# Kernel optimization log

Hardware: AMD Instinct MI355X
Metric: run time of the kernel (lower is better)

## Reference

```python
import jax, jax.numpy as jnp
import numpy as np

B, IN, H, G, WR = 8192, 1024, 1024, 2, 64
UR = [64, 64]


def setup_inputs() -> dict:
    key = jax.random.key(0)
    ks = jax.random.split(key, 9)
    hg = H // G
    return {
        "x": jax.random.normal(ks[0], (B, IN), jnp.float32),
        "h": jax.random.normal(ks[1], (B, H), jnp.float32),
        "c": jax.random.normal(ks[2], (B, H), jnp.float32),
        "u_x": 0.1 * jax.random.normal(ks[3], (IN, WR), jnp.float32),
        "v_x": 0.1 * jax.random.normal(ks[4], (4 * H, WR), jnp.float32),
        "u_h_0": 0.1 * jax.random.normal(ks[5], (G, hg, UR[0]), jnp.float32),
        "v_h_0": 0.1 * jax.random.normal(ks[6], (G, UR[0], 4 * hg), jnp.float32),
        "u_h_1": 0.1 * jax.random.normal(ks[7], (G, hg, UR[1]), jnp.float32),
        "v_h_1": 0.1 * jax.random.normal(ks[8], (G, UR[1], 4 * hg), jnp.float32),
        "bias_x": jnp.ones((1, 4 * H), jnp.float32),
        "bias_h": jnp.ones((1, 4 * H), jnp.float32),
    }


def reference(x, h, c, u_x, v_x, u_h_0, v_h_0, u_h_1, v_h_1, bias_x, bias_h):
    b = h.shape[0]
    hg = H // G
    # input-to-hidden low-rank projection: [B, 4H]
    gx = (x @ u_x) @ v_x.T + bias_x
    xf, xi, xn, xo = jnp.split(gx, 4, axis=1)  # each [B, H]

    hv = h.reshape(b, G, hg)  # [B, G, H/G]
    u_hs = [u_h_0, u_h_1]
    v_hs = [v_h_0, v_h_1]
    acc = None
    for i in range(G):
        # torch code rotates the group index list cumulatively each step:
        # step i uses permutation roll(arange(G), -i)
        perm = np.roll(np.arange(G), -i)
        h_op = hv[:, perm, :]  # [B, G, hg]
        t = jnp.einsum('bgd,gdr->bgr', h_op, u_hs[i])  # [B, G, r_i]
        t = jnp.einsum('bgr,grk->bgk', t, v_hs[i])     # [B, G, 4hg]
        acc = t if acc is None else acc + t

    # chunk along last dim into 4 gates, flatten group dim -> [B, H]
    f_h, i_h, n_h, o_h = [p.reshape(b, H) for p in jnp.split(acc, 4, axis=2)]
    hf, hi, hn, ho = jnp.split(bias_h, 4, axis=1)

    inputgate = jax.nn.sigmoid(xi + hi + i_h)
    forgetgate = jax.nn.sigmoid(xf + hf + f_h)
    outputgate = jax.nn.sigmoid(xo + ho + o_h)
    newgate = jnp.tanh(xn + hn + n_h)
    c_next = forgetgate * c + inputgate * newgate
    h_next = outputgate * jnp.tanh(c_next)
    return (h_next, c_next)
```

## Files before the change

kernel.cpp:

```cpp
#include <hip/hip_runtime.h>
#include <hip/hip_bf16.h>


typedef __bf16 bf16_t;
typedef __bf16 bf16x4 __attribute__((ext_vector_type(4)));
typedef __bf16 bf16x8 __attribute__((ext_vector_type(8)));
typedef float f32x4 __attribute__((ext_vector_type(4)));

#define MFMA16x16x32(a, b, c) __builtin_amdgcn_mfma_f32_16x16x32_bf16((a), (b), (c), 0, 0, 0)

#define TA_OFF 0
#define BX_OFF 5242880
#define BH_OFF 5373952
#define BW_OFF 5636096

__device__ inline float fast_sigmoid(float x) {
  return __builtin_amdgcn_rcpf(1.f + __expf(-x));
}
__device__ inline float fast_tanh(float x) {
  return 2.f * __builtin_amdgcn_rcpf(1.f + __expf(-2.f * x)) - 1.f;
}

__global__ __launch_bounds__(256) void prep_kernel(
    const float* __restrict__ u_x, const float* __restrict__ u_h_0,
    const float* __restrict__ u_h_1, const float* __restrict__ v_h_0,
    const float* __restrict__ v_h_1, const float* __restrict__ v_x,
    bf16_t* __restrict__ Bx, bf16_t* __restrict__ Bh,
    bf16_t* __restrict__ Bw) {
  int o = blockIdx.x * 256 + threadIdx.x;
  if (o < 65536) {
    int j = o & 7, lane = (o >> 3) & 63, kk = (o >> 9) & 31, t = o >> 14;
    int lo = lane & 15, quad = lane >> 4;
    int k = kk * 32 + quad * 8 + j;
    Bx[o] = (bf16_t)u_x[k * 64 + 16 * t + lo];
  } else if (o < 196608) {
    int o2 = o - 65536;
    int j = o2 & 7, lane = (o2 >> 3) & 63, kk = (o2 >> 9) & 15;
    int sub = (o2 >> 13) & 3, s = o2 >> 15;
    int lo = lane & 15, quad = lane >> 4;
    int d = kk * 32 + quad * 8 + j;
    const float* src = (s & 1) ? u_h_1 : u_h_0;
    Bh[o2] = (bf16_t)src[(s >> 1) * 32768 + d * 64 + 16 * sub + lo];
  } else if (o < 983040) {
    int o3 = o - 196608;
    int j = o3 & 7, lane = (o3 >> 3) & 63;
    int chunk = o3 >> 9;
    int ks = chunk % 6, rowt = chunk / 6;
    int gq = rowt >> 3, nt = rowt & 7;
    int lo = lane & 15, quad = lane >> 4;
    int g = gq >> 4, qt = gq & 15;
    int row = 16 * nt + lo;
    int w = row >> 5, ql = row & 31;
    int k = ks * 32 + quad * 8 + j;
    int m = g * 512 + qt * 32 + ql;
    int q = qt * 32 + ql;
    float val;
    if (k < 64)
      val = v_x[(w * 1024 + m) * 64 + k];
    else if (k < 128)
      val = v_h_0[g * 131072 + (k - 64) * 2048 + w * 512 + q];
    else
      val = v_h_1[g * 131072 + (k - 128) * 2048 + w * 512 + q];
    Bw[o3] = (bf16_t)val;
  }
}

__global__ __launch_bounds__(256) void phase1_kernel(
    const float* __restrict__ x, const float* __restrict__ h,
    const bf16_t* __restrict__ Bx, const bf16_t* __restrict__ Bh,
    bf16_t* __restrict__ TA) {
  __shared__ bf16_t z[16][2072];
  __shared__ bf16_t pre[16][328];
  const int b0 = blockIdx.x * 16;
  const int tid = threadIdx.x;
  const int wv = tid >> 6, lane = tid & 63;
  const int lo = lane & 15, quad = lane >> 4;
  const int srow = tid >> 4, sc = tid & 15;

  {
    const float* srcx = x + (size_t)(b0 + srow) * 1024;
    const float* srch = h + (size_t)(b0 + srow) * 1024;
#pragma unroll
    for (int j = 0; j < 16; ++j) {
      int col = sc * 4 + j * 64;
      float4 v = *(const float4*)(srcx + col);
      bf16x4 pk;
      pk[0] = (bf16_t)v.x; pk[1] = (bf16_t)v.y;
      pk[2] = (bf16_t)v.z; pk[3] = (bf16_t)v.w;
      *(bf16x4*)&z[srow][col] = pk;
    }
#pragma unroll
    for (int j = 0; j < 16; ++j) {
      int col = sc * 4 + j * 64;
      float4 v = *(const float4*)(srch + col);
      bf16x4 pk;
      pk[0] = (bf16_t)v.x; pk[1] = (bf16_t)v.y;
      pk[2] = (bf16_t)v.z; pk[3] = (bf16_t)v.w;
      *(bf16x4*)&z[srow][1024 + col] = pk;
    }
  }
  __syncthreads();

  {
    f32x4 accx = {0.f, 0.f, 0.f, 0.f};
    const bf16_t* bx = Bx + ((size_t)(wv * 32) * 64 + lane) * 8;
    for (int kk = 0; kk < 32; ++kk) {
      bf16x8 af = *(const bf16x8*)&z[lo][kk * 32 + quad * 8];
      bf16x8 bfr = *(const bf16x8*)(bx + (size_t)kk * 512);
      accx = MFMA16x16x32(af, bfr, accx);
    }
#pragma unroll
    for (int r = 0; r < 4; ++r) pre[quad * 4 + r][16 * wv + lo] = (bf16_t)accx[r];
  }

  {
    const int hoff = 1024 + ((wv == 1 || wv == 2) ? 512 : 0);
    f32x4 acc[4];
#pragma unroll
    for (int sub = 0; sub < 4; ++sub) acc[sub] = (f32x4){0.f, 0.f, 0.f, 0.f};
    for (int kk = 0; kk < 16; ++kk) {
      bf16x8 af = *(const bf16x8*)&z[lo][hoff + kk * 32 + quad * 8];
#pragma unroll
      for (int sub = 0; sub < 4; ++sub) {
        bf16x8 bfr = *(const bf16x8*)(Bh +
            (((size_t)(wv * 4 + sub) * 16 + kk) * 64 + lane) * 8);
        acc[sub] = MFMA16x16x32(af, bfr, acc[sub]);
      }
    }
#pragma unroll
    for (int sub = 0; sub < 4; ++sub) {
      int n = 64 + wv * 64 + sub * 16 + lo;
#pragma unroll
      for (int r = 0; r < 4; ++r) pre[quad * 4 + r][n] = (bf16_t)acc[sub][r];
    }
  }
  __syncthreads();

#pragma unroll
  for (int it = 0; it < 3; ++it) {
    int slot = it * 256 + tid;
    if (slot < 640) {
      int cc = slot >> 6, ln = slot & 63;
      int llo = ln & 15, lq = ln >> 4;
      bf16x8 v = *(const bf16x8*)&pre[llo][cc * 32 + lq * 8];
      *(bf16x8*)(TA + (((size_t)blockIdx.x * 10 + cc) * 64 + ln) * 8) = v;
    }
  }
}

__global__ __launch_bounds__(256, 3) void phase2_kernel(
    const bf16_t* __restrict__ TA, const bf16_t* __restrict__ Bw,
    const float* __restrict__ bias_x, const float* __restrict__ bias_h,
    const float* __restrict__ c, float* __restrict__ out) {
  __shared__ bf16_t bs[3072 * 8];

  const int b0 = blockIdx.x * 128;
  const int gq = blockIdx.y;
  const int g = gq >> 4, qt = gq & 15;
  const int tid = threadIdx.x;
  const int wv = tid >> 6, lane = tid & 63;
  const int lo = lane & 15, quad = lane >> 4;

  bf16x8 a[2][6];
#pragma unroll
  for (int mt = 0; mt < 2; ++mt) {
    int rt = blockIdx.x * 8 + wv * 2 + mt;
#pragma unroll
    for (int ks = 0; ks < 6; ++ks) {
      int cc = (ks < 2) ? ks : (g * 4 + ks);
      a[mt][ks] = *(const bf16x8*)(TA + (((size_t)rt * 10 + cc) * 64 + lane) * 8);
    }
  }

  {
    const bf16_t* src = Bw + (size_t)gq * 24576;
#pragma unroll
    for (int cch = 0; cch < 12; ++cch) {
      int ch = cch * 256 + tid;
      *(bf16x8*)&bs[(size_t)ch * 8] = *(const bf16x8*)(src + (size_t)ch * 8);
    }
  }

  float cin[2][4][2];
#pragma unroll
  for (int mt = 0; mt < 2; ++mt)
#pragma unroll
    for (int r = 0; r < 4; ++r) {
      int b = b0 + wv * 32 + mt * 16 + quad * 4 + r;
#pragma unroll
      for (int cq = 0; cq < 2; ++cq) {
        int m = g * 512 + qt * 32 + cq * 16 + lo;
        cin[mt][r][cq] = c[(size_t)b * 1024 + m];
      }
    }
  float bsum[4][2];
#pragma unroll
  for (int w = 0; w < 4; ++w)
#pragma unroll
    for (int cq = 0; cq < 2; ++cq) {
      int n = w * 1024 + g * 512 + qt * 32 + cq * 16 + lo;
      bsum[w][cq] = bias_x[n] + bias_h[n];
    }
  __syncthreads();

  f32x4 acc[2][8];
#pragma unroll
  for (int mt = 0; mt < 2; ++mt)
#pragma unroll
    for (int nt = 0; nt < 8; ++nt) acc[mt][nt] = (f32x4){0.f, 0.f, 0.f, 0.f};

#pragma unroll
  for (int nt = 0; nt < 8; ++nt) {
#pragma unroll
    for (int ks = 0; ks < 6; ++ks) {
      bf16x8 bfr = *(const bf16x8*)&bs[(size_t)(((nt * 6 + ks) << 6) + lane) * 8];
      acc[0][nt] = MFMA16x16x32(a[0][ks], bfr, acc[0][nt]);
      acc[1][nt] = MFMA16x16x32(a[1][ks], bfr, acc[1][nt]);
    }
  }

#pragma unroll
  for (int mt = 0; mt < 2; ++mt)
#pragma unroll
    for (int r = 0; r < 4; ++r) {
      int b = b0 + wv * 32 + mt * 16 + quad * 4 + r;
#pragma unroll
      for (int cq = 0; cq < 2; ++cq) {
        int m = g * 512 + qt * 32 + cq * 16 + lo;
        float fv = acc[mt][0 + cq][r] + bsum[0][cq];
        float iv = acc[mt][2 + cq][r] + bsum[1][cq];
        float nv = acc[mt][4 + cq][r] + bsum[2][cq];
        float ov = acc[mt][6 + cq][r] + bsum[3][cq];
        float ig = fast_sigmoid(iv);
        float fg = fast_sigmoid(fv);
        float og = fast_sigmoid(ov);
        float ng = fast_tanh(nv);
        float cn = fg * cin[mt][r][cq] + ig * ng;
        float hn = og * fast_tanh(cn);
        out[(size_t)b * 1024 + m] = hn;
        out[8388608ull + (size_t)b * 1024 + m] = cn;
      }
    }
}

extern "C" void kernel_launch(void* const* d_in, const int* in_sizes, int n_in,
                              void* d_out, int out_size, void* d_ws,
                              size_t ws_size, hipStream_t stream) {
  const float* x = (const float*)d_in[0];
  const float* h = (const float*)d_in[1];
  const float* c = (const float*)d_in[2];
  const float* u_x = (const float*)d_in[3];
  const float* v_x = (const float*)d_in[4];
  const float* u_h_0 = (const float*)d_in[5];
  const float* v_h_0 = (const float*)d_in[6];
  const float* u_h_1 = (const float*)d_in[7];
  const float* v_h_1 = (const float*)d_in[8];
  const float* bias_x = (const float*)d_in[9];
  const float* bias_h = (const float*)d_in[10];

  char* ws = (char*)d_ws;
  bf16_t* TA = (bf16_t*)(ws + TA_OFF);
  bf16_t* Bx = (bf16_t*)(ws + BX_OFF);
  bf16_t* Bh = (bf16_t*)(ws + BH_OFF);
  bf16_t* Bw = (bf16_t*)(ws + BW_OFF);

  prep_kernel<<<3840, 256, 0, stream>>>(u_x, u_h_0, u_h_1, v_h_0, v_h_1, v_x,
                                        Bx, Bh, Bw);
  phase1_kernel<<<512, 256, 0, stream>>>(x, h, Bx, Bh, TA);
  phase2_kernel<<<dim3(64, 32), 256, 0, stream>>>(TA, Bw, bias_x, bias_h, c,
                                                  (float*)d_out);
}
```

Before: 192.3 us.

## Vectorize weight prep, widen phase1 to 8 waves, drop LDS staging in phase2

The prep kernel now has each thread build a full bf16x8 fragment and write it as one vector, using fewer threads and wider stores. Phase1 doubles its block to 512 threads and spreads the hidden-projection MFMA tiles across 8 waves for better balance. Phase2 drops its shared-memory B staging and the barrier, reads weight fragments straight from global memory (relying on cache), and raises its occupancy hint to 4. Direct global reads may add latency to the MFMA loop, since several blocks share the same weights.

```diff
diff --git a/kernel.cpp b/kernel.cpp
--- a/kernel.cpp
+++ b/kernel.cpp
@@ -27,45 +27,62 @@
     const float* __restrict__ v_h_1, const float* __restrict__ v_x,
     bf16_t* __restrict__ Bx, bf16_t* __restrict__ Bh,
     bf16_t* __restrict__ Bw) {
-  int o = blockIdx.x * 256 + threadIdx.x;
-  if (o < 65536) {
-    int j = o & 7, lane = (o >> 3) & 63, kk = (o >> 9) & 31, t = o >> 14;
-    int lo = lane & 15, quad = lane >> 4;
-    int k = kk * 32 + quad * 8 + j;
-    Bx[o] = (bf16_t)u_x[k * 64 + 16 * t + lo];
-  } else if (o < 196608) {
-    int o2 = o - 65536;
-    int j = o2 & 7, lane = (o2 >> 3) & 63, kk = (o2 >> 9) & 15;
-    int sub = (o2 >> 13) & 3, s = o2 >> 15;
-    int lo = lane & 15, quad = lane >> 4;
-    int d = kk * 32 + quad * 8 + j;
-    const float* src = (s & 1) ? u_h_1 : u_h_0;
-    Bh[o2] = (bf16_t)src[(s >> 1) * 32768 + d * 64 + 16 * sub + lo];
-  } else if (o < 983040) {
-    int o3 = o - 196608;
-    int j = o3 & 7, lane = (o3 >> 3) & 63;
-    int chunk = o3 >> 9;
+  int t = blockIdx.x * 256 + threadIdx.x;
+  int lane = t & 63;
+  int lo = lane & 15, quad = lane >> 4;
+  if (t < 8192) {
+    int kk = (t >> 6) & 31, tt = t >> 11;
+    int k0 = kk * 32 + quad * 8;
+    const float* src = u_x + 16 * tt + lo;
+    bf16x8 v;
+#pragma unroll
+    for (int j = 0; j < 8; ++j) v[j] = (bf16_t)src[(size_t)(k0 + j) * 64];
+    *(bf16x8*)(Bx + (size_t)t * 8) = v;
+  } else if (t < 24576) {
+    int o2 = t - 8192;
+    int kk = (o2 >> 6) & 15, sub = (o2 >> 10) & 3, s = o2 >> 12;
+    int d0 = kk * 32 + quad * 8;
+    const float* src =
+        ((s & 1) ? u_h_1 : u_h_0) + (size_t)(s >> 1) * 32768 + 16 * sub + lo;
+    bf16x8 v;
+#pragma unroll
+    for (int j = 0; j < 8; ++j) v[j] = (bf16_t)src[(size_t)(d0 + j) * 64];
+    *(bf16x8*)(Bh + (size_t)o2 * 8) = v;
+  } else {
+    int t3 = t - 24576;
+    int chunk = t3 >> 6;
     int ks = chunk % 6, rowt = chunk / 6;
     int gq = rowt >> 3, nt = rowt & 7;
-    int lo = lane & 15, quad = lane >> 4;
-    int g = gq >> 4, qt = gq & 15;
+    int gg = gq >> 4, qt = gq & 15;
     int row = 16 * nt + lo;
     int w = row >> 5, ql = row & 31;
-    int k = ks * 32 + quad * 8 + j;
-    int m = g * 512 + qt * 32 + ql;
+    int k0 = ks * 32 + quad * 8;
+    int m = gg * 512 + qt * 32 + ql;
     int q = qt * 32 + ql;
-    float val;
-    if (k < 64)
-      val = v_x[(w * 1024 + m) * 64 + k];
-    else if (k < 128)
-      val = v_h_0[g * 131072 + (k - 64) * 2048 + w * 512 + q];
-    else
-      val = v_h_1[g * 131072 + (k - 128) * 2048 + w * 512 + q];
-    Bw[o3] = (bf16_t)val;
-  }
-}
-
-__global__ __launch_bounds__(256) void phase1_kernel(
+    bf16x8 v;
+    if (ks < 2) {
+      const float4* p = (const float4*)(v_x + (size_t)(w * 1024 + m) * 64 + k0);
+      float4 va = p[0], vb = p[1];
+      v[0] = (bf16_t)va.x; v[1] = (bf16_t)va.y;
+      v[2] = (bf16_t)va.z; v[3] = (bf16_t)va.w;
+      v[4] = (bf16_t)vb.x; v[5] = (bf16_t)vb.y;
+      v[6] = (bf16_t)vb.z; v[7] = (bf16_t)vb.w;
+    } else if (ks < 4) {
+      const float* src = v_h_0 + (size_t)gg * 131072 +
+                         (size_t)(k0 - 64) * 2048 + w * 512 + q;
+#pragma unroll
+      for (int j = 0; j < 8; ++j) v[j] = (bf16_t)src[(size_t)j * 2048];
+    } else {
+      const float* src = v_h_1 + (size_t)gg * 131072 +
+                         (size_t)(k0 - 128) * 2048 + w * 512 + q;
+#pragma unroll
+      for (int j = 0; j < 8; ++j) v[j] = (bf16_t)src[(size_t)j * 2048];
+    }
+    *(bf16x8*)(Bw + (size_t)t3 * 8) = v;
+  }
+}
+
+__global__ __launch_bounds__(512) void phase1_kernel(
     const float* __restrict__ x, const float* __restrict__ h,
     const bf16_t* __restrict__ Bx, const bf16_t* __restrict__ Bh,
     bf16_t* __restrict__ TA) {
@@ -75,33 +92,31 @@
   const int tid = threadIdx.x;
   const int wv = tid >> 6, lane = tid & 63;
   const int lo = lane & 15, quad = lane >> 4;
-  const int srow = tid >> 4, sc = tid & 15;
+  const int srow = tid >> 5, sc = tid & 31;
 
   {
-    const float* srcx = x + (size_t)(b0 + srow) * 1024;
-    const float* srch = h + (size_t)(b0 + srow) * 1024;
-#pragma unroll
-    for (int j = 0; j < 16; ++j) {
-      int col = sc * 4 + j * 64;
-      float4 v = *(const float4*)(srcx + col);
+    const float* srcx = x + (size_t)(b0 + srow) * 1024 + sc * 4;
+    const float* srch = h + (size_t)(b0 + srow) * 1024 + sc * 4;
+#pragma unroll
+    for (int j = 0; j < 8; ++j) {
+      float4 v = *(const float4*)(srcx + j * 128);
       bf16x4 pk;
       pk[0] = (bf16_t)v.x; pk[1] = (bf16_t)v.y;
       pk[2] = (bf16_t)v.z; pk[3] = (bf16_t)v.w;
-      *(bf16x4*)&z[srow][col] = pk;
-    }
-#pragma unroll
-    for (int j = 0; j < 16; ++j) {
-      int col = sc * 4 + j * 64;
-      float4 v = *(const float4*)(srch + col);
+      *(bf16x4*)&z[srow][sc * 4 + j * 128] = pk;
+    }
+#pragma unroll
+    for (int j = 0; j < 8; ++j) {
+      float4 v = *(const float4*)(srch + j * 128);
       bf16x4 pk;
       pk[0] = (bf16_t)v.x; pk[1] = (bf16_t)v.y;
       pk[2] = (bf16_t)v.z; pk[3] = (bf16_t)v.w;
-      *(bf16x4*)&z[srow][1024 + col] = pk;
+      *(bf16x4*)&z[srow][1024 + sc * 4 + j * 128] = pk;
     }
   }
   __syncthreads();
 
-  {
+  if (wv < 4) {
     f32x4 accx = {0.f, 0.f, 0.f, 0.f};
     const bf16_t* bx = Bx + ((size_t)(wv * 32) * 64 + lane) * 8;
     for (int kk = 0; kk < 32; ++kk) {
@@ -111,34 +126,49 @@
     }
 #pragma unroll
     for (int r = 0; r < 4; ++r) pre[quad * 4 + r][16 * wv + lo] = (bf16_t)accx[r];
-  }
-
-  {
-    const int hoff = 1024 + ((wv == 1 || wv == 2) ? 512 : 0);
-    f32x4 acc[4];
-#pragma unroll
-    for (int sub = 0; sub < 4; ++sub) acc[sub] = (f32x4){0.f, 0.f, 0.f, 0.f};
+
+    const int u = 12 + wv;
+    f32x4 acch = {0.f, 0.f, 0.f, 0.f};
+    const bf16_t* bh = Bh + ((size_t)(u * 16) * 64 + lane) * 8;
     for (int kk = 0; kk < 16; ++kk) {
-      bf16x8 af = *(const bf16x8*)&z[lo][hoff + kk * 32 + quad * 8];
-#pragma unroll
-      for (int sub = 0; sub < 4; ++sub) {
-        bf16x8 bfr = *(const bf16x8*)(Bh +
-            (((size_t)(wv * 4 + sub) * 16 + kk) * 64 + lane) * 8);
-        acc[sub] = MFMA16x16x32(af, bfr, acc[sub]);
+      bf16x8 af = *(const bf16x8*)&z[lo][1024 + kk * 32 + quad * 8];
+      bf16x8 bfr = *(const bf16x8*)(bh + (size_t)kk * 512);
+      acch = MFMA16x16x32(af, bfr, acch);
+    }
+#pragma unroll
+    for (int r = 0; r < 4; ++r)
+      pre[quad * 4 + r][64 + u * 16 + lo] = (bf16_t)acch[r];
+  } else {
+    const int ub = (wv - 4) * 3;
+    f32x4 acc[3];
+#pragma unroll
+    for (int i = 0; i < 3; ++i) acc[i] = (f32x4){0.f, 0.f, 0.f, 0.f};
+    int hoffA[3];
+#pragma unroll
+    for (int i = 0; i < 3; ++i) {
+      int s = (ub + i) >> 2;
+      hoffA[i] = 1024 + ((s == 1 || s == 2) ? 512 : 0);
+    }
+    const bf16_t* bh = Bh + ((size_t)(ub * 16) * 64 + lane) * 8;
+    for (int kk = 0; kk < 16; ++kk) {
+#pragma unroll
+      for (int i = 0; i < 3; ++i) {
+        bf16x8 af = *(const bf16x8*)&z[lo][hoffA[i] + kk * 32 + quad * 8];
+        bf16x8 bfr = *(const bf16x8*)(bh + ((size_t)i * 16 + kk) * 512);
+        acc[i] = MFMA16x16x32(af, bfr, acc[i]);
       }
     }
 #pragma unroll
-    for (int sub = 0; sub < 4; ++sub) {
-      int n = 64 + wv * 64 + sub * 16 + lo;
-#pragma unroll
-      for (int r = 0; r < 4; ++r) pre[quad * 4 + r][n] = (bf16_t)acc[sub][r];
-    }
+    for (int i = 0; i < 3; ++i)
+#pragma unroll
+      for (int r = 0; r < 4; ++r)
+        pre[quad * 4 + r][64 + (ub + i) * 16 + lo] = (bf16_t)acc[i][r];
   }
   __syncthreads();
 
 #pragma unroll
-  for (int it = 0; it < 3; ++it) {
-    int slot = it * 256 + tid;
+  for (int it = 0; it < 2; ++it) {
+    int slot = it * 512 + tid;
     if (slot < 640) {
       int cc = slot >> 6, ln = slot & 63;
       int llo = ln & 15, lq = ln >> 4;
@@ -148,12 +178,10 @@
   }
 }
 
-__global__ __launch_bounds__(256, 3) void phase2_kernel(
+__global__ __launch_bounds__(256, 4) void phase2_kernel(
     const bf16_t* __restrict__ TA, const bf16_t* __restrict__ Bw,
     const float* __restrict__ bias_x, const float* __restrict__ bias_h,
     const float* __restrict__ c, float* __restrict__ out) {
-  __shared__ bf16_t bs[3072 * 8];
-
   const int b0 = blockIdx.x * 128;
   const int gq = blockIdx.y;
   const int g = gq >> 4, qt = gq & 15;
@@ -172,15 +200,32 @@
     }
   }
 
-  {
-    const bf16_t* src = Bw + (size_t)gq * 24576;
-#pragma unroll
-    for (int cch = 0; cch < 12; ++cch) {
-      int ch = cch * 256 + tid;
-      *(bf16x8*)&bs[(size_t)ch * 8] = *(const bf16x8*)(src + (size_t)ch * 8);
-    }
-  }
-
+  const bf16_t* bw = Bw + (size_t)gq * 24576 + (size_t)lane * 8;
+
+  f32x4 acc[2][8];
+#pragma unroll
+  for (int mt = 0; mt < 2; ++mt)
+#pragma unroll
+    for (int nt = 0; nt < 8; ++nt) acc[mt][nt] = (f32x4){0.f, 0.f, 0.f, 0.f};
+
+#pragma unroll
+  for (int nt = 0; nt < 8; ++nt) {
+#pragma unroll
+    for (int ks = 0; ks < 6; ++ks) {
+      bf16x8 bfr = *(const bf16x8*)(bw + (size_t)((nt * 6 + ks) << 6) * 8);
+      acc[0][nt] = MFMA16x16x32(a[0][ks], bfr, acc[0][nt]);
+      acc[1][nt] = MFMA16x16x32(a[1][ks], bfr, acc[1][nt]);
+    }
+  }
+
+  float bsum[4][2];
+#pragma unroll
+  for (int w = 0; w < 4; ++w)
+#pragma unroll
+    for (int cq = 0; cq < 2; ++cq) {
+      int n = w * 1024 + g * 512 + qt * 32 + cq * 16 + lo;
+      bsum[w][cq] = bias_x[n] + bias_h[n];
+    }
   float cin[2][4][2];
 #pragma unroll
   for (int mt = 0; mt < 2; ++mt)
@@ -193,31 +238,6 @@
         cin[mt][r][cq] = c[(size_t)b * 1024 + m];
       }
     }
-  float bsum[4][2];
-#pragma unroll
-  for (int w = 0; w < 4; ++w)
-#pragma unroll
-    for (int cq = 0; cq < 2; ++cq) {
-      int n = w * 1024 + g * 512 + qt * 32 + cq * 16 + lo;
-      bsum[w][cq] = bias_x[n] + bias_h[n];
-    }
-  __syncthreads();
-
-  f32x4 acc[2][8];
-#pragma unroll
-  for (int mt = 0; mt < 2; ++mt)
-#pragma unroll
-    for (int nt = 0; nt < 8; ++nt) acc[mt][nt] = (f32x4){0.f, 0.f, 0.f, 0.f};
-
-#pragma unroll
-  for (int nt = 0; nt < 8; ++nt) {
-#pragma unroll
-    for (int ks = 0; ks < 6; ++ks) {
-      bf16x8 bfr = *(const bf16x8*)&bs[(size_t)(((nt * 6 + ks) << 6) + lane) * 8];
-      acc[0][nt] = MFMA16x16x32(a[0][ks], bfr, acc[0][nt]);
-      acc[1][nt] = MFMA16x16x32(a[1][ks], bfr, acc[1][nt]);
-    }
-  }
 
 #pragma unroll
   for (int mt = 0; mt < 2; ++mt)
@@ -264,9 +284,9 @@
   bf16_t* Bh = (bf16_t*)(ws + BH_OFF);
   bf16_t* Bw = (bf16_t*)(ws + BW_OFF);
 
-  prep_kernel<<<3840, 256, 0, stream>>>(u_x, u_h_0, u_h_1, v_h_0, v_h_1, v_x,
-                                        Bx, Bh, Bw);
-  phase1_kernel<<<512, 256, 0, stream>>>(x, h, Bx, Bh, TA);
+  prep_kernel<<<480, 256, 0, stream>>>(u_x, u_h_0, u_h_1, v_h_0, v_h_1, v_x,
+                                       Bx, Bh, Bw);
+  phase1_kernel<<<512, 512, 0, stream>>>(x, h, Bx, Bh, TA);
   phase2_kernel<<<dim3(64, 32), 256, 0, stream>>>(TA, Bw, bias_x, bias_h, c,
                                                   (float*)d_out);
 }
```

New measurement: 210.6 us. +9.5%, slower.
